# Kernel optimization log

Hardware: AMD Instinct MI355X
Metric: run time of the kernel (lower is better)

The kernel has to match this reference:

```python
import jax, jax.numpy as jnp
import numpy as np

B, L, H, E = 32, 128, 768, 64


def setup_inputs() -> dict:
    key = jax.random.key(0)
    ks = jax.random.split(key, 9)
    bert = jax.random.normal(ks[0], (B, L, H), jnp.float32)
    dep = jax.random.normal(ks[1], (B, L, L, E), jnp.float32)
    adj = jax.random.bernoulli(ks[2], 0.06, (B, L, L)).astype(jnp.int32)
    adj = adj.at[:, :, L - 1].set(0)  # avoid torch.roll wrap pairing edge case
    asp_start = jax.random.randint(ks[3], (B,), 1, L // 2)
    span = jax.random.randint(ks[4], (B,), 0, 4)
    asp_end = jnp.minimum(asp_start + span, L - 2)
    sc = 1.0 / np.sqrt(H).astype(np.float32)
    Wz = jax.random.normal(ks[5], (H, H), jnp.float32) * sc
    bz = jnp.zeros((H,), jnp.float32)
    wa = jax.random.normal(ks[6], (2 * H + E,), jnp.float32) * sc
    ba = jnp.zeros((), jnp.float32)
    Wf = jax.random.normal(ks[7], (H, H + E), jnp.float32) * sc
    Wh = jax.random.normal(ks[8], (H, 2 * H), jnp.float32) * sc
    return dict(bert_hidden_states=bert, dep_type_adj=dep, deprel_adj=adj,
                asp_start=asp_start, asp_end=asp_end,
                Wz=Wz, bz=bz, wa=wa, ba=ba, Wf=Wf, Wh=Wh)


def _forward(bert, dep, adj, asp_start, asp_end, Wz, bz, wa, ba, Wf, Wh):
    # z = z_linear(bert); zs[b, j] = z[b, j+1] (rolled-mask offset: adjacency idx j -> token j+1)
    z = bert @ Wz.T + bz
    zs = jnp.roll(z, -1, axis=1)                      # [B,L,H]
    wa_i, wa_j, wa_e = wa[:H], wa[H:2 * H], wa[2 * H:]
    s_i = zs @ wa_i                                    # [B,L] current-aspect term
    s_j = zs @ wa_j                                    # [B,L] neighbor term
    s_e = jnp.einsum('bije,e->bij', dep, wa_e)         # [B,L,L] dep-embed term
    score = jax.nn.leaky_relu(s_i[:, :, None] + s_j[:, None, :] + s_e + ba, 0.01)
    nb_mask = adj > 0                                  # [B,L,L]
    attn = jax.nn.softmax(jnp.where(nb_mask, score, -1e9), axis=-1)
    attn = jnp.where(nb_mask, attn, 0.0)
    # dep_type_fusion([neighbor, dep]) = zs @ Wf_z^T + dep @ Wf_e^T; weighted sum over j
    A = zs @ Wf[:, :H].T                               # [B,L,H]
    D = jnp.einsum('bij,bije->bie', attn, dep)         # [B,L,E]
    neighbor_repr = jnp.einsum('bij,bjh->bih', attn, A) + D @ Wf[:, H:].T  # [B,L,H]
    # w_h([neighbor_repr, current_asp_repr])
    temp = neighbor_repr @ Wh[:, :H].T + zs @ Wh[:, H:].T                   # [B,L,H]
    pos = jnp.arange(L)
    asp_valid = (pos[None, :] >= asp_start[:, None]) & (pos[None, :] <= asp_end[:, None])
    upd = asp_valid & nb_mask.any(-1)                  # update only aspects with >=1 neighbor
    # result for adjacency index i is written to token position i+1
    out = jnp.where(jnp.roll(upd, 1, axis=1)[:, :, None], jnp.roll(temp, 1, axis=1), bert)
    return out


def reference(bert_hidden_states, dep_type_adj, deprel_adj, asp_start, asp_end, Wz, bz, wa, ba, Wf, Wh):
    return _forward(bert_hidden_states, dep_type_adj, deprel_adj, asp_start, asp_end,
                    Wz, bz, wa, ba, Wf, Wh)
```

## Files before the change

kernel.cpp:

```cpp
#include <hip/hip_runtime.h>
#include <math.h>

#define NB 32
#define NL 128
#define NH 768
#define NE 64

#define OFF_ASLOT   32784
#define OFF_AIDX    49168
#define OFF_NASP    49680
#define OFF_AJCNT   49808
#define OFF_AJIDX   50320
#define OFF_RMAP    148624
#define OFF_BZD     155280
#define OFF_YB      155296
#define OFF_DG      548512
#define OFF_YP      581280
#define OFF_ZSAP    2154144
#define OFF_NBR     3727008
#define OFF_VIP     6872736
#define OFF_VJP     6897312

__global__ __launch_bounds__(256) void kA(
    const int* __restrict__ adj, const int* __restrict__ asp_s, const int* __restrict__ asp_e,
    const float* __restrict__ Wz, const float* __restrict__ wa, const float* __restrict__ bz,
    int* __restrict__ aspect_slot, int* __restrict__ aspect_idx, int* __restrict__ nasp,
    int* __restrict__ aj_cnt, int* __restrict__ aj_idx, int* __restrict__ row_map,
    float* __restrict__ viP, float* __restrict__ vjP, float* __restrict__ bzd) {
  int blk = blockIdx.x, tid = threadIdx.x;
  if (blk < 32) {
    int b = blk;
    __shared__ int asp_flag[128];
    __shared__ int s_aidx[4];
    __shared__ int s_nasp;
    if (tid < 128) {
      const int* arow = adj + ((size_t)(b * 128 + tid)) * 128;
      int any = 0;
      for (int j = 0; j < 128; j += 4) {
        int4 v = *(const int4*)(arow + j);
        any |= v.x | v.y | v.z | v.w;
      }
      int s0 = asp_s[b], e0 = asp_e[b];
      asp_flag[tid] = (tid >= s0 && tid <= e0 && any > 0) ? 1 : 0;
      aspect_slot[b * 128 + tid] = -1;
    }
    if (tid >= 128 && tid < 132) row_map[b * 4 + (tid - 128)] = b * 128;
    __syncthreads();
    if (tid == 0) {
      int n = 0;
      for (int i = 0; i < 128; ++i)
        if (asp_flag[i] && n < 4) s_aidx[n++] = i;
      s_nasp = n;
      nasp[b] = n;
    }
    __syncthreads();
    int w = tid >> 6, l = tid & 63;
    if (w < s_nasp) {
      int a = s_aidx[w];
      if (l == 0) {
        aspect_idx[b * 4 + w] = a;
        aspect_slot[b * 128 + a] = w;
        row_map[b * 4 + w] = b * 128 + a;
      }
      const int* ar = adj + ((size_t)(b * 128 + a)) * 128;
      int v0 = (ar[l] > 0) ? 1 : 0;
      int v1 = (ar[l + 64] > 0) ? 1 : 0;
      unsigned long long m0 = __ballot(v0);
      unsigned long long m1 = __ballot(v1);
      unsigned long long below = (1ull << l) - 1ull;
      int c0 = __popcll(m0 & below);
      int c1 = __popcll(m0) + __popcll(m1 & below);
      int* dst = aj_idx + (size_t)(b * 4 + w) * 128;
      if (v0) dst[c0] = l;
      if (v1) dst[c1] = l + 64;
      if (l == 0) aj_cnt[b * 4 + w] = __popcll(m0) + __popcll(m1);
    }
  } else if (blk < 56) {
    int idx = blk - 32;
    int kb = idx % 3, hb = idx / 3;
    int k = kb * 256 + tid;
    int h0 = hb * 96;
    float ai = 0.f, aj = 0.f;
#pragma unroll 8
    for (int h = h0; h < h0 + 96; ++h) {
      float w = Wz[(size_t)h * 768 + k];
      ai += w * wa[h];
      aj += w * wa[768 + h];
    }
    viP[hb * 768 + k] = ai;
    vjP[hb * 768 + k] = aj;
  } else {
    if (tid < 64) {
      float bi = 0.f, bj = 0.f;
#pragma unroll
      for (int q = 0; q < 12; ++q) {
        float bv = bz[q * 64 + tid];
        bi += bv * wa[q * 64 + tid];
        bj += bv * wa[768 + q * 64 + tid];
      }
#pragma unroll
      for (int d = 32; d; d >>= 1) { bi += __shfl_xor(bi, d, 64); bj += __shfl_xor(bj, d, 64); }
      if (tid == 0) { bzd[0] = bi; bzd[1] = bj; }
    }
  }
}

__global__ __launch_bounds__(256) void kB(
    const float* __restrict__ dep, const float* __restrict__ bert,
    const float* __restrict__ wa, const float* __restrict__ ba,
    const float* __restrict__ viP, const float* __restrict__ vjP, const float* __restrict__ bzd,
    const float* __restrict__ Wz, const float* __restrict__ bz,
    const int* __restrict__ nasp, const int* __restrict__ aspect_idx,
    const int* __restrict__ aj_cnt, const int* __restrict__ aj_idx,
    const int* __restrict__ aspect_slot, const int* __restrict__ row_map,
    float* __restrict__ YB, float* __restrict__ DG, float* __restrict__ zsap,
    float* __restrict__ out) {
  int blk = blockIdx.x, tid = threadIdx.x;
  if (blk < 32) {
    int b = blk;
    int na = nasp[b];
    if (na == 0) return;
    __shared__ float vis[768];
    __shared__ float vjs[768];
    __shared__ float att[4][128];
    __shared__ float sjs[4][128];
    __shared__ float sis[4];
    __shared__ int jl[4][128];
    __shared__ int aidx[4];
    __shared__ int ajc[4];
    __shared__ float wae[64];
    if (tid < 4) { aidx[tid] = aspect_idx[b * 4 + tid]; ajc[tid] = aj_cnt[b * 4 + tid]; }
    if (tid < 64) wae[tid] = wa[1536 + tid];
    for (int q = tid; q < 512; q += 256) jl[q >> 7][q & 127] = aj_idx[b * 512 + q];
    for (int q = tid; q < 768; q += 256) {
      float a = 0.f, c = 0.f;
#pragma unroll
      for (int hb = 0; hb < 8; ++hb) { a += viP[hb * 768 + q]; c += vjP[hb * 768 + q]; }
      vis[q] = a;
      vjs[q] = c;
    }
    __syncthreads();
    int w = tid >> 6, l = tid & 63;
    float bzd0 = bzd[0], bzd1 = bzd[1];
    int offs[5];
    {
      int o = 0;
      for (int w2 = 0; w2 < 4; ++w2) { offs[w2] = o; if (w2 < na) o += 1 + ajc[w2]; }
      offs[4] = o;
    }
    for (int p = w; p < offs[4]; p += 4) {
      int w2 = 0;
      if (p >= offs[1]) w2 = 1;
      if (p >= offs[2]) w2 = 2;
      if (p >= offs[3]) w2 = 3;
      int idx = p - offs[w2];
      int row = (idx == 0) ? aidx[w2] : jl[w2][idx - 1];
      const float* br = bert + (size_t)(b * 128 + ((row + 1) & 127)) * 768;
      float acc = 0.f;
      if (idx == 0) {
#pragma unroll
        for (int q = 0; q < 12; ++q) acc += br[q * 64 + l] * vis[q * 64 + l];
      } else {
#pragma unroll
        for (int q = 0; q < 12; ++q) acc += br[q * 64 + l] * vjs[q * 64 + l];
      }
#pragma unroll
      for (int d = 32; d; d >>= 1) acc += __shfl_xor(acc, d, 64);
      if (l == 0) {
        if (idx == 0) sis[w2] = acc + bzd0;
        else sjs[w2][idx - 1] = acc + bzd1;
      }
    }
    __syncthreads();
    if (w >= na) return;
    int a = aidx[w], cj = ajc[w];
    float sib = sis[w] + ba[0];
    const float* depa = dep + ((size_t)(b * 128 + a)) * 128 * 64;
    float sc0 = -INFINITY, sc1 = -INFINITY;
    for (int t = l; t < cj; t += 64) {
      int j = jl[w][t];
      const float4* dp = (const float4*)(depa + (size_t)j * 64);
      float se = 0.f;
#pragma unroll
      for (int q = 0; q < 16; ++q) {
        float4 v = dp[q];
        se += v.x * wae[4 * q] + v.y * wae[4 * q + 1] + v.z * wae[4 * q + 2] + v.w * wae[4 * q + 3];
      }
      float sc = sib + sjs[w][t] + se;
      sc = (sc >= 0.f) ? sc : 0.01f * sc;
      if (t < 64) sc0 = sc; else sc1 = sc;
    }
    float mx = fmaxf(sc0, sc1);
#pragma unroll
    for (int d = 32; d; d >>= 1) mx = fmaxf(mx, __shfl_xor(mx, d, 64));
    float p0 = expf(sc0 - mx), p1 = expf(sc1 - mx);
    float sm = p0 + p1;
#pragma unroll
    for (int d = 32; d; d >>= 1) sm += __shfl_xor(sm, d, 64);
    float inv = 1.f / sm;
    if (l < cj) att[w][l] = p0 * inv;
    if (l + 64 < cj) att[w][l + 64] = p1 * inv;
    float y[12];
#pragma unroll
    for (int q = 0; q < 12; ++q) y[q] = 0.f;
    float dacc = 0.f;
    for (int t = 0; t < cj; ++t) {
      float at = att[w][t];
      int j = jl[w][t];
      const float* br = bert + (size_t)(b * 128 + ((j + 1) & 127)) * 768;
#pragma unroll
      for (int q = 0; q < 12; ++q) y[q] += at * br[q * 64 + l];
      dacc += at * depa[(size_t)j * 64 + l];
    }
    float* yr = YB + (size_t)(b * 4 + w) * 768;
#pragma unroll
    for (int q = 0; q < 12; ++q) yr[q * 64 + l] = y[q];
    DG[(b * 4 + w) * 64 + l] = dacc;
  } else if (blk < 416) {
    int idx = blk - 32;
    int kc = idx & 3, hc = (idx >> 2) % 3, bx = idx / 12;
    int s0 = bx * 4;
    __shared__ float Xs[4][192];
    if (tid < 192) {
      int r = tid / 48, c = tid - r * 48;
      int zrow = row_map[s0 + r];
      int bb = zrow >> 7, ii = zrow & 127;
      const float4* src = (const float4*)(bert + ((size_t)(bb * 128) + ((ii + 1) & 127)) * 768) + kc * 48;
      ((float4*)Xs[r])[c] = src[c];
    }
    __syncthreads();
    int h = hc * 256 + tid;
    const float4* wp = (const float4*)(Wz + (size_t)h * 768) + kc * 48;
    float accA[4] = {};
    float accB[4] = {};
#pragma unroll 6
    for (int k4 = 0; k4 < 24; ++k4) {
      float4 w0 = wp[k4];
      float4 w1 = wp[k4 + 24];
#pragma unroll
      for (int r = 0; r < 4; ++r) {
        float4 x0 = ((const float4*)Xs[r])[k4];
        float4 x1 = ((const float4*)Xs[r])[k4 + 24];
        accA[r] += x0.x * w0.x + x0.y * w0.y + x0.z * w0.z + x0.w * w0.w;
        accB[r] += x1.x * w1.x + x1.y * w1.y + x1.z * w1.z + x1.w * w1.w;
      }
    }
    float bzv = (kc == 0) ? bz[h] : 0.f;
#pragma unroll
    for (int r = 0; r < 4; ++r)
      zsap[((size_t)kc * 128 + s0 + r) * 768 + h] = accA[r] + accB[r] + bzv;
  } else {
    int idx = (blk - 416) * 256 + tid;
    int row = idx / 192;
    int b = row >> 7, i = row & 127;
    int slot = (i > 0) ? aspect_slot[b * 128 + i - 1] : -1;
    float4 v = make_float4(0.f, 0.f, 0.f, 0.f);
    if (slot < 0) v = ((const float4*)bert)[idx];
    ((float4*)out)[idx] = v;
  }
}

__global__ __launch_bounds__(256) void kC(
    const float* __restrict__ YB, const float* __restrict__ DG, const float* __restrict__ zsap,
    const float* __restrict__ Wz, const float* __restrict__ bz,
    const float* __restrict__ Wf, const float* __restrict__ Wh,
    const int* __restrict__ row_map, const int* __restrict__ nasp,
    float* __restrict__ yp, float* __restrict__ NBR, float* __restrict__ out) {
  int blk = blockIdx.x, tid = threadIdx.x;
  __shared__ float Xs[4][384];
  if (blk < 384) {
    int kc = blk & 3, hc = (blk >> 2) % 3, bx = blk / 12;
    int s0 = bx * 4;
    if (tid < 192) {
      int r = tid / 48, c = tid - r * 48;
      const float4* src = (const float4*)(YB + (size_t)(s0 + r) * 768) + kc * 48;
      ((float4*)Xs[r])[c] = src[c];
    }
    __syncthreads();
    int h = hc * 256 + tid;
    const float4* wp = (const float4*)(Wz + (size_t)h * 768) + kc * 48;
    float accA[4] = {};
    float accB[4] = {};
#pragma unroll 6
    for (int k4 = 0; k4 < 24; ++k4) {
      float4 w0 = wp[k4];
      float4 w1 = wp[k4 + 24];
#pragma unroll
      for (int r = 0; r < 4; ++r) {
        float4 x0 = ((const float4*)Xs[r])[k4];
        float4 x1 = ((const float4*)Xs[r])[k4 + 24];
        accA[r] += x0.x * w0.x + x0.y * w0.y + x0.z * w0.z + x0.w * w0.w;
        accB[r] += x1.x * w1.x + x1.y * w1.y + x1.z * w1.z + x1.w * w1.w;
      }
    }
    float bzv = (kc == 0) ? bz[h] : 0.f;
#pragma unroll
    for (int r = 0; r < 4; ++r)
      yp[((size_t)kc * 128 + s0 + r) * 768 + h] = accA[r] + accB[r] + bzv;
  } else if (blk < 576) {
    int idx = blk - 384;
    int kc2 = idx & 1, nc = (idx >> 1) % 3, g = idx / 6;
#pragma unroll
    for (int r = 0; r < 4; ++r) {
      if (tid < 96) {
        int row = g * 4 + r;
        int Q = kc2 * 96 + tid;
        float4 p0 = *((const float4*)(zsap + (size_t)row * 768) + Q);
        float4 p1 = *((const float4*)(zsap + ((size_t)128 + row) * 768) + Q);
        float4 p2 = *((const float4*)(zsap + ((size_t)256 + row) * 768) + Q);
        float4 p3 = *((const float4*)(zsap + ((size_t)384 + row) * 768) + Q);
        ((float4*)Xs[r])[tid] = make_float4(p0.x + p1.x + p2.x + p3.x, p0.y + p1.y + p2.y + p3.y,
                                            p0.z + p1.z + p2.z + p3.z, p0.w + p1.w + p2.w + p3.w);
      }
    }
    __syncthreads();
    int h = nc * 256 + tid;
    float acc[4] = {};
    const float4* wp = (const float4*)(Wh + (size_t)h * 1536 + 768 + kc2 * 384);
#pragma unroll 4
    for (int k4 = 0; k4 < 96; ++k4) {
      float4 wv = wp[k4];
#pragma unroll
      for (int r = 0; r < 4; ++r) {
        float4 xv = ((const float4*)Xs[r])[k4];
        acc[r] += xv.x * wv.x + xv.y * wv.y + xv.z * wv.z + xv.w * wv.w;
      }
    }
#pragma unroll
    for (int r = 0; r < 4; ++r) {
      int row = g * 4 + r;
      int b = row >> 2, s = row & 3;
      if (s < nasp[b]) {
        int orow = row_map[row] + 1;
        atomicAdd(&out[(size_t)orow * 768 + h], acc[r]);
      }
    }
  } else {
    int idx = blk - 576;
    int nc = idx % 3, g = idx / 3;
    if (tid < 64) {
      int r = tid / 16, c = tid - r * 16;
      ((float4*)Xs[r])[c] = *((const float4*)(DG + (size_t)(g * 4 + r) * 64) + c);
    }
    __syncthreads();
    int h = nc * 256 + tid;
    float acc[4] = {};
    const float4* wp = (const float4*)(Wf + (size_t)h * 832 + 768);
#pragma unroll
    for (int k4 = 0; k4 < 16; ++k4) {
      float4 wv = wp[k4];
#pragma unroll
      for (int r = 0; r < 4; ++r) {
        float4 xv = ((const float4*)Xs[r])[k4];
        acc[r] += xv.x * wv.x + xv.y * wv.y + xv.z * wv.z + xv.w * wv.w;
      }
    }
#pragma unroll
    for (int r = 0; r < 4; ++r)
      NBR[(size_t)(g * 4 + r) * 768 + h] = acc[r];
  }
}

__global__ __launch_bounds__(256) void kD(
    const float* __restrict__ yp, const float* __restrict__ Wf,
    float* __restrict__ NBR) {
  int blk = blockIdx.x, tid = threadIdx.x;
  int kc = blk & 3, nc = (blk >> 2) % 3, g = blk / 12;
  __shared__ float Xs[4][192];
  if (tid < 192) {
    int r = tid / 48, c = tid - r * 48;
    int row = g * 4 + r;
    int Q = kc * 48 + c;
    float4 p0 = *((const float4*)(yp + (size_t)row * 768) + Q);
    float4 p1 = *((const float4*)(yp + ((size_t)128 + row) * 768) + Q);
    float4 p2 = *((const float4*)(yp + ((size_t)256 + row) * 768) + Q);
    float4 p3 = *((const float4*)(yp + ((size_t)384 + row) * 768) + Q);
    ((float4*)Xs[r])[c] = make_float4(p0.x + p1.x + p2.x + p3.x, p0.y + p1.y + p2.y + p3.y,
                                      p0.z + p1.z + p2.z + p3.z, p0.w + p1.w + p2.w + p3.w);
  }
  __syncthreads();
  int h = nc * 256 + tid;
  float acc[4] = {};
  const float4* wp = (const float4*)(Wf + (size_t)h * 832 + kc * 192);
#pragma unroll 4
  for (int k4 = 0; k4 < 48; ++k4) {
    float4 wv = wp[k4];
#pragma unroll
    for (int r = 0; r < 4; ++r) {
      float4 xv = ((const float4*)Xs[r])[k4];
      acc[r] += xv.x * wv.x + xv.y * wv.y + xv.z * wv.z + xv.w * wv.w;
    }
  }
#pragma unroll
  for (int r = 0; r < 4; ++r)
    atomicAdd(&NBR[(size_t)(g * 4 + r) * 768 + h], acc[r]);
}

__global__ __launch_bounds__(256) void kE(
    const float* __restrict__ NBR, const float* __restrict__ Wh,
    const int* __restrict__ row_map, const int* __restrict__ nasp,
    float* __restrict__ out) {
  int blk = blockIdx.x, tid = threadIdx.x;
  int kc = blk & 1, nc = (blk >> 1) % 3, g = blk / 6;
  __shared__ float Xs[4][384];
#pragma unroll
  for (int r = 0; r < 4; ++r) {
    if (tid < 96)
      ((float4*)Xs[r])[tid] = *((const float4*)(NBR + (size_t)(g * 4 + r) * 768 + kc * 384) + tid);
  }
  __syncthreads();
  int h = nc * 256 + tid;
  float acc[4] = {};
  const float4* wp = (const float4*)(Wh + (size_t)h * 1536 + kc * 384);
#pragma unroll 4
  for (int k4 = 0; k4 < 96; ++k4) {
    float4 wv = wp[k4];
#pragma unroll
    for (int r = 0; r < 4; ++r) {
      float4 xv = ((const float4*)Xs[r])[k4];
      acc[r] += xv.x * wv.x + xv.y * wv.y + xv.z * wv.z + xv.w * wv.w;
    }
  }
#pragma unroll
  for (int r = 0; r < 4; ++r) {
    int row = g * 4 + r;
    int b = row >> 2, s = row & 3;
    if (s < nasp[b]) {
      int orow = row_map[row] + 1;
      atomicAdd(&out[(size_t)orow * 768 + h], acc[r]);
    }
  }
}

extern "C" void kernel_launch(void* const* d_in, const int* in_sizes, int n_in,
                              void* d_out, int out_size, void* d_ws, size_t ws_size,
                              hipStream_t stream) {
  const float* bert = (const float*)d_in[0];
  const float* dep  = (const float*)d_in[1];
  const int*   adj  = (const int*)d_in[2];
  const int*   asps = (const int*)d_in[3];
  const int*   aspe = (const int*)d_in[4];
  const float* Wz   = (const float*)d_in[5];
  const float* bz   = (const float*)d_in[6];
  const float* wa   = (const float*)d_in[7];
  const float* ba   = (const float*)d_in[8];
  const float* Wf   = (const float*)d_in[9];
  const float* Wh   = (const float*)d_in[10];
  float* out = (float*)d_out;
  char* ws = (char*)d_ws;

  int*   aspect_slot = (int*)(ws + OFF_ASLOT);
  int*   aspect_idx  = (int*)(ws + OFF_AIDX);
  int*   nasp        = (int*)(ws + OFF_NASP);
  int*   aj_cnt      = (int*)(ws + OFF_AJCNT);
  int*   aj_idx      = (int*)(ws + OFF_AJIDX);
  int*   row_map     = (int*)(ws + OFF_RMAP);
  float* bzd         = (float*)(ws + OFF_BZD);
  float* YB          = (float*)(ws + OFF_YB);
  float* DG          = (float*)(ws + OFF_DG);
  float* yp          = (float*)(ws + OFF_YP);
  float* zsap        = (float*)(ws + OFF_ZSAP);
  float* NBR         = (float*)(ws + OFF_NBR);
  float* viP         = (float*)(ws + OFF_VIP);
  float* vjP         = (float*)(ws + OFF_VJP);

  kA<<<57, 256, 0, stream>>>(adj, asps, aspe, Wz, wa, bz,
                             aspect_slot, aspect_idx, nasp, aj_cnt, aj_idx, row_map,
                             viP, vjP, bzd);
  kB<<<3488, 256, 0, stream>>>(dep, bert, wa, ba, viP, vjP, bzd, Wz, bz,
                               nasp, aspect_idx, aj_cnt, aj_idx, aspect_slot, row_map,
                               YB, DG, zsap, out);
  kC<<<672, 256, 0, stream>>>(YB, DG, zsap, Wz, bz, Wf, Wh, row_map, nasp, yp, NBR, out);
  kD<<<384, 256, 0, stream>>>(yp, Wf, NBR);
  kE<<<192, 256, 0, stream>>>(NBR, Wh, row_map, nasp, out);
}
```

Measured before the change: 93.81 us.

## Move output copy into first kernel and split Wh GEMV blocks finer

The bulk copy of bert into out, with zeros on rows that get updated, now runs inside kA as 4096 extra blocks. Each block recomputes the row's update flag directly from adj instead of reading aspect_slot, so the copy no longer waits behind kB. The Wh-based matvecs in kC and kE now split K into 4 chunks of 192 instead of 2 of 384, which doubles the block count to raise parallelism. The cost is more atomicAdds onto out and NBR, and out is now written in kA, before kC and kE add into it.

```diff
diff --git a/kernel.cpp b/kernel.cpp
--- a/kernel.cpp
+++ b/kernel.cpp
@@ -24,9 +24,11 @@
 __global__ __launch_bounds__(256) void kA(
     const int* __restrict__ adj, const int* __restrict__ asp_s, const int* __restrict__ asp_e,
     const float* __restrict__ Wz, const float* __restrict__ wa, const float* __restrict__ bz,
+    const float* __restrict__ bert,
     int* __restrict__ aspect_slot, int* __restrict__ aspect_idx, int* __restrict__ nasp,
     int* __restrict__ aj_cnt, int* __restrict__ aj_idx, int* __restrict__ row_map,
-    float* __restrict__ viP, float* __restrict__ vjP, float* __restrict__ bzd) {
+    float* __restrict__ viP, float* __restrict__ vjP, float* __restrict__ bzd,
+    float* __restrict__ out) {
   int blk = blockIdx.x, tid = threadIdx.x;
   if (blk < 32) {
     int b = blk;
@@ -89,7 +91,7 @@
     }
     viP[hb * 768 + k] = ai;
     vjP[hb * 768 + k] = aj;
-  } else {
+  } else if (blk == 56) {
     if (tid < 64) {
       float bi = 0.f, bj = 0.f;
 #pragma unroll
@@ -101,6 +103,28 @@
 #pragma unroll
       for (int d = 32; d; d >>= 1) { bi += __shfl_xor(bi, d, 64); bj += __shfl_xor(bj, d, 64); }
       if (tid == 0) { bzd[0] = bi; bzd[1] = bj; }
+    }
+  } else {
+    int row = blk - 57;
+    int b = row >> 7, i = row & 127;
+    __shared__ int s_upd;
+    if (tid == 0) s_upd = 0;
+    __syncthreads();
+    if (i > 0) {
+      int ip = i - 1;
+      int s0 = asp_s[b], e0 = asp_e[b];
+      if (ip >= s0 && ip <= e0 && tid < 64) {
+        const int2* ar = (const int2*)(adj + ((size_t)(b * 128 + ip)) * 128);
+        int2 v = ar[tid];
+        unsigned long long m = __ballot((v.x | v.y) != 0);
+        if (tid == 0 && m != 0ull) s_upd = 1;
+      }
+    }
+    __syncthreads();
+    if (tid < 192) {
+      float4 v = make_float4(0.f, 0.f, 0.f, 0.f);
+      if (!s_upd) v = ((const float4*)bert)[(size_t)row * 192 + tid];
+      ((float4*)out)[(size_t)row * 192 + tid] = v;
     }
   }
 }
@@ -112,9 +136,8 @@
     const float* __restrict__ Wz, const float* __restrict__ bz,
     const int* __restrict__ nasp, const int* __restrict__ aspect_idx,
     const int* __restrict__ aj_cnt, const int* __restrict__ aj_idx,
-    const int* __restrict__ aspect_slot, const int* __restrict__ row_map,
-    float* __restrict__ YB, float* __restrict__ DG, float* __restrict__ zsap,
-    float* __restrict__ out) {
+    const int* __restrict__ row_map,
+    float* __restrict__ YB, float* __restrict__ DG, float* __restrict__ zsap) {
   int blk = blockIdx.x, tid = threadIdx.x;
   if (blk < 32) {
     int b = blk;
@@ -216,7 +239,7 @@
 #pragma unroll
     for (int q = 0; q < 12; ++q) yr[q * 64 + l] = y[q];
     DG[(b * 4 + w) * 64 + l] = dacc;
-  } else if (blk < 416) {
+  } else {
     int idx = blk - 32;
     int kc = idx & 3, hc = (idx >> 2) % 3, bx = idx / 12;
     int s0 = bx * 4;
@@ -249,14 +272,6 @@
 #pragma unroll
     for (int r = 0; r < 4; ++r)
       zsap[((size_t)kc * 128 + s0 + r) * 768 + h] = accA[r] + accB[r] + bzv;
-  } else {
-    int idx = (blk - 416) * 256 + tid;
-    int row = idx / 192;
-    int b = row >> 7, i = row & 127;
-    int slot = (i > 0) ? aspect_slot[b * 128 + i - 1] : -1;
-    float4 v = make_float4(0.f, 0.f, 0.f, 0.f);
-    if (slot < 0) v = ((const float4*)bert)[idx];
-    ((float4*)out)[idx] = v;
   }
 }
 
@@ -267,7 +282,7 @@
     const int* __restrict__ row_map, const int* __restrict__ nasp,
     float* __restrict__ yp, float* __restrict__ NBR, float* __restrict__ out) {
   int blk = blockIdx.x, tid = threadIdx.x;
-  __shared__ float Xs[4][384];
+  __shared__ float Xs[4][192];
   if (blk < 384) {
     int kc = blk & 3, hc = (blk >> 2) % 3, bx = blk / 12;
     int s0 = bx * 4;
@@ -297,28 +312,26 @@
 #pragma unroll
     for (int r = 0; r < 4; ++r)
       yp[((size_t)kc * 128 + s0 + r) * 768 + h] = accA[r] + accB[r] + bzv;
-  } else if (blk < 576) {
+  } else if (blk < 768) {
     int idx = blk - 384;
-    int kc2 = idx & 1, nc = (idx >> 1) % 3, g = idx / 6;
-#pragma unroll
-    for (int r = 0; r < 4; ++r) {
-      if (tid < 96) {
-        int row = g * 4 + r;
-        int Q = kc2 * 96 + tid;
-        float4 p0 = *((const float4*)(zsap + (size_t)row * 768) + Q);
-        float4 p1 = *((const float4*)(zsap + ((size_t)128 + row) * 768) + Q);
-        float4 p2 = *((const float4*)(zsap + ((size_t)256 + row) * 768) + Q);
-        float4 p3 = *((const float4*)(zsap + ((size_t)384 + row) * 768) + Q);
-        ((float4*)Xs[r])[tid] = make_float4(p0.x + p1.x + p2.x + p3.x, p0.y + p1.y + p2.y + p3.y,
-                                            p0.z + p1.z + p2.z + p3.z, p0.w + p1.w + p2.w + p3.w);
-      }
+    int kc2 = idx & 3, nc = (idx >> 2) % 3, g = idx / 12;
+    if (tid < 192) {
+      int r = tid / 48, c = tid - r * 48;
+      int row = g * 4 + r;
+      int Q = kc2 * 48 + c;
+      float4 p0 = *((const float4*)(zsap + (size_t)row * 768) + Q);
+      float4 p1 = *((const float4*)(zsap + ((size_t)128 + row) * 768) + Q);
+      float4 p2 = *((const float4*)(zsap + ((size_t)256 + row) * 768) + Q);
+      float4 p3 = *((const float4*)(zsap + ((size_t)384 + row) * 768) + Q);
+      ((float4*)Xs[r])[c] = make_float4(p0.x + p1.x + p2.x + p3.x, p0.y + p1.y + p2.y + p3.y,
+                                        p0.z + p1.z + p2.z + p3.z, p0.w + p1.w + p2.w + p3.w);
     }
     __syncthreads();
     int h = nc * 256 + tid;
     float acc[4] = {};
-    const float4* wp = (const float4*)(Wh + (size_t)h * 1536 + 768 + kc2 * 384);
+    const float4* wp = (const float4*)(Wh + (size_t)h * 1536 + 768 + kc2 * 192);
 #pragma unroll 4
-    for (int k4 = 0; k4 < 96; ++k4) {
+    for (int k4 = 0; k4 < 48; ++k4) {
       float4 wv = wp[k4];
 #pragma unroll
       for (int r = 0; r < 4; ++r) {
@@ -336,7 +349,7 @@
       }
     }
   } else {
-    int idx = blk - 576;
+    int idx = blk - 768;
     int nc = idx % 3, g = idx / 3;
     if (tid < 64) {
       int r = tid / 16, c = tid - r * 16;
@@ -401,19 +414,18 @@
     const int* __restrict__ row_map, const int* __restrict__ nasp,
     float* __restrict__ out) {
   int blk = blockIdx.x, tid = threadIdx.x;
-  int kc = blk & 1, nc = (blk >> 1) % 3, g = blk / 6;
-  __shared__ float Xs[4][384];
-#pragma unroll
-  for (int r = 0; r < 4; ++r) {
-    if (tid < 96)
-      ((float4*)Xs[r])[tid] = *((const float4*)(NBR + (size_t)(g * 4 + r) * 768 + kc * 384) + tid);
+  int kc = blk & 3, nc = (blk >> 2) % 3, g = blk / 12;
+  __shared__ float Xs[4][192];
+  if (tid < 192) {
+    int r = tid / 48, c = tid - r * 48;
+    ((float4*)Xs[r])[c] = *((const float4*)(NBR + (size_t)(g * 4 + r) * 768 + kc * 192) + c);
   }
   __syncthreads();
   int h = nc * 256 + tid;
   float acc[4] = {};
-  const float4* wp = (const float4*)(Wh + (size_t)h * 1536 + kc * 384);
+  const float4* wp = (const float4*)(Wh + (size_t)h * 1536 + kc * 192);
 #pragma unroll 4
-  for (int k4 = 0; k4 < 96; ++k4) {
+  for (int k4 = 0; k4 < 48; ++k4) {
     float4 wv = wp[k4];
 #pragma unroll
     for (int r = 0; r < 4; ++r) {
@@ -464,13 +476,13 @@
   float* viP         = (float*)(ws + OFF_VIP);
   float* vjP         = (float*)(ws + OFF_VJP);
 
-  kA<<<57, 256, 0, stream>>>(adj, asps, aspe, Wz, wa, bz,
-                             aspect_slot, aspect_idx, nasp, aj_cnt, aj_idx, row_map,
-                             viP, vjP, bzd);
-  kB<<<3488, 256, 0, stream>>>(dep, bert, wa, ba, viP, vjP, bzd, Wz, bz,
-                               nasp, aspect_idx, aj_cnt, aj_idx, aspect_slot, row_map,
-                               YB, DG, zsap, out);
-  kC<<<672, 256, 0, stream>>>(YB, DG, zsap, Wz, bz, Wf, Wh, row_map, nasp, yp, NBR, out);
+  kA<<<4153, 256, 0, stream>>>(adj, asps, aspe, Wz, wa, bz, bert,
+                               aspect_slot, aspect_idx, nasp, aj_cnt, aj_idx, row_map,
+                               viP, vjP, bzd, out);
+  kB<<<416, 256, 0, stream>>>(dep, bert, wa, ba, viP, vjP, bzd, Wz, bz,
+                              nasp, aspect_idx, aj_cnt, aj_idx, row_map,
+                              YB, DG, zsap);
+  kC<<<864, 256, 0, stream>>>(YB, DG, zsap, Wz, bz, Wf, Wh, row_map, nasp, yp, NBR, out);
   kD<<<384, 256, 0, stream>>>(yp, Wf, NBR);
-  kE<<<192, 256, 0, stream>>>(NBR, Wh, row_map, nasp, out);
-}
+  kE<<<384, 256, 0, stream>>>(NBR, Wh, row_map, nasp, out);
+}
```

Measured after the change: 86.80 us (median of 3 runs). -7.5%, faster.
